# Kernel tuning notes

Measured on AMD Instinct MI355X. Metric: run time of the kernel, lower is better.

The kernel has to match this reference:

```python
import jax, jax.numpy as jnp
import numpy as np

RATIO_DENSE = 0.95   # ratio_th[-2] used for dense matching at conv5_2
RATIO_REFINE = 0.9   # ratio_th[k] used by refine_points
EPS = 1e-8
NEIGHBORS = jnp.array([[0, 0], [0, 1], [1, 0], [1, 1]])  # (x, y) offsets


def setup_inputs() -> dict:
    key = jax.random.key(0)
    k1, k2, k3, k4 = jax.random.split(key, 4)
    return {
        'map_A': jax.random.normal(k1, (1, 512, 96, 96), dtype=jnp.float32),
        'map_B': jax.random.normal(k2, (1, 512, 96, 96), dtype=jnp.float32),
        'act_A': jax.random.normal(k3, (1, 512, 192, 192), dtype=jnp.float32),
        'act_B': jax.random.normal(k4, (1, 512, 192, 192), dtype=jnp.float32),
    }


def _mnn_ratio_mask(sim, ratio):
    """Mutual-NN + ratio-test. sim: [N1, N2] cosine similarities.
    Returns nn12 [N1] (best match in B for each A) and boolean mask [N1]."""
    s12, i12 = jax.lax.top_k(sim, 2)            # [N1, 2]
    d12 = 2.0 - 2.0 * s12                       # cosine sim -> squared L2 dist
    r12 = d12[:, 0] / (d12[:, 1] + EPS)
    nn12 = i12[:, 0]
    s21, i21 = jax.lax.top_k(sim.T, 2)          # [N2, 2]
    d21 = 2.0 - 2.0 * s21
    r21 = d21[:, 0] / (d21[:, 1] + EPS)
    nn21 = i21[:, 0]
    ids1 = jnp.arange(sim.shape[0])
    mask = (ids1 == nn21[nn12]) & (r12 <= ratio) & (r21[nn12] <= ratio)
    return nn12, mask


def reference(map_A, map_B, act_A, act_B):
    ch = map_A.shape[1]
    hA, wA = map_A.shape[2], map_A.shape[3]
    hB, wB = map_B.shape[2], map_B.shape[3]

    # ---- dense_feature_matching (padded / masked form) ----
    d1 = map_A.reshape(ch, -1).T               # [N1, ch]
    d1 = d1 / jnp.linalg.norm(d1, axis=1, keepdims=True)
    d2 = map_B.reshape(ch, -1).T               # [N2, ch]
    d2 = d2 / jnp.linalg.norm(d2, axis=1, keepdims=True)
    sim = d1 @ d2.T                            # [N1, N2], the big one
    nn12, valid = _mnn_ratio_mask(sim, RATIO_DENSE)

    idx = jnp.arange(hA * wA)
    yA, xA = jnp.divmod(idx, wA)
    yB, xB = jnp.divmod(nn12, wB)
    border = ((xA == 0) | (xA == wA - 1) | (yA == 0) | (yA == hA - 1) |
              (xB == 0) | (xB == wB - 1) | (yB == 0) | (yB == hB - 1))
    valid = valid & ~border
    # pad invalid points to (0,0) so refine gathers stay in-bounds
    pA = jnp.stack([jnp.where(valid, xA, 0), jnp.where(valid, yA, 0)])  # [2, P]
    pB = jnp.stack([jnp.where(valid, xB, 0), jnp.where(valid, yB, 0)])

    # ---- refine_points (fully vectorized gather-dot-topk over all P points) ----
    dA = act_A[0] / jnp.sqrt(jnp.sum(act_A[0] ** 2, axis=0, keepdims=True))
    dB = act_B[0] / jnp.sqrt(jnp.sum(act_B[0] ** 2, axis=0, keepdims=True))
    pA2 = pA * 2
    pB2 = pB * 2
    P = pA.shape[1]

    gAx = pA2[0][:, None] + NEIGHBORS[:, 0][None, :]   # [P, 4]
    gAy = pA2[1][:, None] + NEIGHBORS[:, 1][None, :]
    gBx = pB2[0][:, None] + NEIGHBORS[:, 0][None, :]
    gBy = pB2[1][:, None] + NEIGHBORS[:, 1][None, :]
    actAg = dA[:, gAy, gAx]                            # [ch, P, 4]
    actBg = dB[:, gBy, gBx]                            # [ch, P, 4]
    scores = jnp.einsum('cpi,cpj->pij', actAg, actBg)  # [P, 4, 4]

    sA, mA = jax.lax.top_k(scores, 2)                  # [P, 4, 2]
    sA = 2.0 - 2.0 * sA
    ratio_A2B = sA[..., 0] / (sA[..., 1] + EPS)        # [P, 4]
    match_A2B = mA[..., 0]
    score_A2B = sA[..., 0]

    sB, mB = jax.lax.top_k(jnp.swapaxes(scores, 1, 2), 2)
    sB = 2.0 - 2.0 * sB
    ratio_B2A = sB[..., 0] / (sB[..., 1] + EPS)
    match_B2A = mB[..., 0]

    ar = jnp.arange(P)
    ind_A = (ar[:, None] * 4 + match_A2B).reshape(-1)  # [P*4]
    ind_B = (ar[:, None] * 4 + match_B2A).reshape(-1)
    ind = jnp.arange(P * 4)
    mask = (jnp.minimum(ratio_A2B, ratio_B2A) < RATIO_REFINE) & \
           (ind_B[ind_A] == ind).reshape(P, 4)

    # drop the two worst (largest-distance) neighbor candidates per point
    score_masked = jnp.where(mask, score_A2B, 5.0)
    _, discard = jax.lax.top_k(score_masked, 2)
    mask = mask.at[ar, discard[:, 0]].set(False)
    mask = mask.at[ar, discard[:, 1]].set(False)
    mask = mask & valid[:, None]

    refined_A = jnp.stack([gAx, gAy])                                   # [2, P, 4]
    rBx = pB2[0][:, None] + NEIGHBORS[:, 0][match_A2B]
    rBy = pB2[1][:, None] + NEIGHBORS[:, 1][match_A2B]
    refined_B = jnp.stack([rBx, rBy])                                   # [2, P, 4]

    return refined_A, refined_B, mask, scores
```

## Files before the change

### kernel.cpp

```cpp
#include <hip/hip_runtime.h>
#include <stdint.h>

#define CH 512
#define W1 96
#define P1 (W1*W1)
#define W2 192
#define P2 (W2*W2)
#define TILE 128
#define NT (P1/TILE)
#define BK 32
#define EPSF 1e-8f
#define RDENSE 0.95f
#define RREFINE 0.9f

typedef __attribute__((ext_vector_type(8))) short bf16x8_t;
typedef __attribute__((ext_vector_type(4))) float f32x4_t;

__device__ __forceinline__ unsigned enc_f32(float f){
  unsigned u = __float_as_uint(f);
  return (u & 0x80000000u) ? ~u : (u | 0x80000000u);
}
__device__ __forceinline__ float dec_f32(unsigned e){
  unsigned u = (e & 0x80000000u) ? (e & 0x7FFFFFFFu) : ~e;
  return __uint_as_float(u);
}
__device__ __forceinline__ unsigned long long packVI(float v, int idx){
  return (((unsigned long long)enc_f32(v)) << 32) | (unsigned)(~(unsigned)idx);
}
__device__ __forceinline__ float packedVal(unsigned long long p){ return dec_f32((unsigned)(p >> 32)); }
__device__ __forceinline__ int packedIdx(unsigned long long p){ return (int)(~(unsigned)(p & 0xFFFFFFFFull)); }
__device__ __forceinline__ void merge2(unsigned long long &b, unsigned long long &s, unsigned long long c){
  if (c > b){ s = b; b = c; } else if (c > s){ s = c; }
}

__device__ __forceinline__ unsigned short f2bf(float f){
  unsigned u = __float_as_uint(f);
  unsigned r = (u + 0x7FFFu + ((u >> 16) & 1u)) >> 16;
  return (unsigned short)r;
}

__device__ __forceinline__ void gload16(const void* g, void* l){
  __builtin_amdgcn_global_load_lds(
      (const __attribute__((address_space(1))) unsigned int*)g,
      (__attribute__((address_space(3))) unsigned int*)l, 16, 0, 0);
}

__global__ void desc_norm(const float* __restrict__ mA, const float* __restrict__ mB,
                          float* __restrict__ inv1, float* __restrict__ inv2){
  int p = blockIdx.x * blockDim.x + threadIdx.x;
  const float* m = (p < P1) ? mA : mB;
  float* o = (p < P1) ? inv1 : inv2;
  int pix = (p < P1) ? p : p - P1;
  float s = 0.f;
  for (int c = 0; c < CH; ++c){ float v = m[c*P1 + pix]; s += v*v; }
  o[pix] = 1.0f / sqrtf(s);
}

__global__ void act_norm(const float* __restrict__ aA, const float* __restrict__ aB,
                         float* __restrict__ invA, float* __restrict__ invB){
  int p = blockIdx.x * blockDim.x + threadIdx.x;
  const float* m = (p < P2) ? aA : aB;
  float* o = (p < P2) ? invA : invB;
  int pix = (p < P2) ? p : p - P2;
  float s = 0.f;
  for (int c = 0; c < CH; ++c){ float v = m[c*P2 + pix]; s += v*v; }
  o[pix] = 1.0f / sqrtf(s);
}

__global__ __launch_bounds__(256)
void prep_split(const float* __restrict__ src, const float* __restrict__ inv,
                unsigned short* __restrict__ hi, unsigned short* __restrict__ lo){
  __shared__ float tile[64][65];
  const int pixBase = blockIdx.x * 64;
  const int chBase  = blockIdx.y * 64;
  const int t = threadIdx.x;
  #pragma unroll
  for (int rep = 0; rep < 16; ++rep){
    int idx = rep*256 + t;
    int c = idx >> 6, p = idx & 63;
    tile[c][p] = src[(chBase + c)*P1 + pixBase + p];
  }
  __syncthreads();
  const int p = t >> 2, cg = (t & 3) * 16;
  const float iv = inv[pixBase + p];
  unsigned short hbuf[16], lbuf[16];
  #pragma unroll
  for (int j = 0; j < 16; ++j){
    float v = tile[cg + j][p] * iv;
    unsigned short h = f2bf(v);
    float hv = __uint_as_float((unsigned)h << 16);
    unsigned short l2 = f2bf(v - hv);
    hbuf[j] = h; lbuf[j] = l2;
  }
  size_t off = (size_t)(pixBase + p) * CH + chBase + cg;
  *(uint4*)(hi + off)     = ((const uint4*)hbuf)[0];
  *(uint4*)(hi + off + 8) = ((const uint4*)hbuf)[1];
  *(uint4*)(lo + off)     = ((const uint4*)lbuf)[0];
  *(uint4*)(lo + off + 8) = ((const uint4*)lbuf)[1];
}

__global__ __launch_bounds__(256, 2)
void sim_mfma(const unsigned short* __restrict__ Ah, const unsigned short* __restrict__ Al,
              const unsigned short* __restrict__ Bh, const unsigned short* __restrict__ Bl,
              unsigned long long* __restrict__ rowCand,
              unsigned long long* __restrict__ colCand){
  __shared__ unsigned short ldsT[4][TILE*BK];
  __shared__ unsigned long long rowScr[TILE][2][2];
  __shared__ unsigned long long colScr[TILE][2][2];

  const int nwg = NT*NT;
  int bid = blockIdx.x;
  int swz = (bid & 7) * (nwg >> 3) + (bid >> 3);
  const int rt = swz / NT, ct = swz % NT;
  const int rBase = rt * TILE, cBase = ct * TILE;

  const int t = threadIdx.x;
  const int w = t >> 6, lane = t & 63;
  const int wr = w >> 1, wc = w & 1;
  const int l15 = lane & 15, lj = lane >> 4;

  const unsigned short* panel = (w == 0) ? (Ah + (size_t)rBase*CH)
                              : (w == 1) ? (Al + (size_t)rBase*CH)
                              : (w == 2) ? (Bh + (size_t)cBase*CH)
                                         : (Bl + (size_t)cBase*CH);
  int srcOff[8];
  #pragma unroll
  for (int i = 0; i < 8; ++i){
    int slot = i*64 + lane;
    int row = slot >> 2, chkp = slot & 3;
    int chk = chkp ^ ((row >> 1) & 3);
    srcOff[i] = row * (CH*2) + chk * 16;
  }

  f32x4_t acc[4][4];
  #pragma unroll
  for (int i = 0; i < 4; ++i)
    #pragma unroll
    for (int j = 0; j < 4; ++j)
      #pragma unroll
      for (int r = 0; r < 4; ++r) acc[i][j][r] = 0.f;

  int aOff[4], bOff[4];
  #pragma unroll
  for (int mi = 0; mi < 4; ++mi){
    int rA = wr*64 + mi*16 + l15;
    aOff[mi] = rA*BK + ((lj ^ ((rA >> 1) & 3)) << 3);
  }
  #pragma unroll
  for (int ni = 0; ni < 4; ++ni){
    int rB = wc*64 + ni*16 + l15;
    bOff[ni] = rB*BK + ((lj ^ ((rB >> 1) & 3)) << 3);
  }

  for (int k0 = 0; k0 < CH; k0 += BK){
    const char* pbase = (const char*)panel + k0*2;
    unsigned short* mylds = &ldsT[w][0];
    #pragma unroll
    for (int i = 0; i < 8; ++i)
      gload16(pbase + srcOff[i], mylds + i*512);
    __syncthreads();

    bf16x8_t ah[4], al[4], bh[4], bl[4];
    #pragma unroll
    for (int mi = 0; mi < 4; ++mi){
      ah[mi] = *(const bf16x8_t*)&ldsT[0][aOff[mi]];
      al[mi] = *(const bf16x8_t*)&ldsT[1][aOff[mi]];
    }
    #pragma unroll
    for (int ni = 0; ni < 4; ++ni){
      bh[ni] = *(const bf16x8_t*)&ldsT[2][bOff[ni]];
      bl[ni] = *(const bf16x8_t*)&ldsT[3][bOff[ni]];
    }
    #pragma unroll
    for (int mi = 0; mi < 4; ++mi)
      #pragma unroll
      for (int ni = 0; ni < 4; ++ni){
        acc[mi][ni] = __builtin_amdgcn_mfma_f32_16x16x32_bf16(ah[mi], bh[ni], acc[mi][ni], 0, 0, 0);
        acc[mi][ni] = __builtin_amdgcn_mfma_f32_16x16x32_bf16(ah[mi], bl[ni], acc[mi][ni], 0, 0, 0);
        acc[mi][ni] = __builtin_amdgcn_mfma_f32_16x16x32_bf16(al[mi], bh[ni], acc[mi][ni], 0, 0, 0);
      }
    __syncthreads();
  }

  #pragma unroll
  for (int mi = 0; mi < 4; ++mi){
    #pragma unroll
    for (int reg = 0; reg < 4; ++reg){
      unsigned long long b = 0ull, s = 0ull;
      #pragma unroll
      for (int ni = 0; ni < 4; ++ni){
        int col = cBase + wc*64 + ni*16 + l15;
        merge2(b, s, packVI(acc[mi][ni][reg], col));
      }
      #pragma unroll
      for (int m = 1; m < 16; m <<= 1){
        unsigned long long ob = __shfl_xor(b, m, 64);
        unsigned long long os = __shfl_xor(s, m, 64);
        merge2(b, s, ob); merge2(b, s, os);
      }
      if (l15 == 0){
        int rowLoc = wr*64 + mi*16 + lj*4 + reg;
        rowScr[rowLoc][wc][0] = b; rowScr[rowLoc][wc][1] = s;
      }
    }
  }
  #pragma unroll
  for (int ni = 0; ni < 4; ++ni){
    unsigned long long b = 0ull, s = 0ull;
    #pragma unroll
    for (int mi = 0; mi < 4; ++mi)
      #pragma unroll
      for (int reg = 0; reg < 4; ++reg){
        int row = rBase + wr*64 + mi*16 + lj*4 + reg;
        merge2(b, s, packVI(acc[mi][ni][reg], row));
      }
    #pragma unroll
    for (int m = 16; m < 64; m <<= 1){
      unsigned long long ob = __shfl_xor(b, m, 64);
      unsigned long long os = __shfl_xor(s, m, 64);
      merge2(b, s, ob); merge2(b, s, os);
    }
    if (lj == 0){
      int colLoc = wc*64 + ni*16 + l15;
      colScr[colLoc][wr][0] = b; colScr[colLoc][wr][1] = s;
    }
  }
  __syncthreads();
  if (t < TILE){
    unsigned long long b = 0ull, s = 0ull;
    merge2(b, s, rowScr[t][0][0]); merge2(b, s, rowScr[t][0][1]);
    merge2(b, s, rowScr[t][1][0]); merge2(b, s, rowScr[t][1][1]);
    rowCand[((long long)ct*P1 + rBase + t)*2 + 0] = b;
    rowCand[((long long)ct*P1 + rBase + t)*2 + 1] = s;
  } else {
    int c = t - TILE;
    unsigned long long b = 0ull, s = 0ull;
    merge2(b, s, colScr[c][0][0]); merge2(b, s, colScr[c][0][1]);
    merge2(b, s, colScr[c][1][0]); merge2(b, s, colScr[c][1][1]);
    colCand[((long long)rt*P1 + cBase + c)*2 + 0] = b;
    colCand[((long long)rt*P1 + cBase + c)*2 + 1] = s;
  }
}

__global__ void merge_cand(const unsigned long long* __restrict__ cand,
                           unsigned long long* __restrict__ top,
                           unsigned long long* __restrict__ sec){
  int p = blockIdx.x * blockDim.x + threadIdx.x;
  unsigned long long b = 0ull, s = 0ull;
  for (int tile = 0; tile < NT; ++tile){
    merge2(b, s, cand[((long long)tile*P1 + p)*2 + 0]);
    merge2(b, s, cand[((long long)tile*P1 + p)*2 + 1]);
  }
  top[p] = b; sec[p] = s;
}

__global__ void match_k(const unsigned long long* __restrict__ rowTop,
                        const unsigned long long* __restrict__ rowSec,
                        const unsigned long long* __restrict__ colTop,
                        const unsigned long long* __restrict__ colSec,
                        int4* __restrict__ pts, int* __restrict__ validArr){
  int p = blockIdx.x * blockDim.x + threadIdx.x;
  unsigned long long rT = rowTop[p], rS = rowSec[p];
  float s0 = packedVal(rT), s1 = packedVal(rS);
  int nn12 = packedIdx(rT);
  float r12 = (2.f - 2.f*s0) / (2.f - 2.f*s1 + EPSF);
  unsigned long long cT = colTop[nn12], cS = colSec[nn12];
  int nn21 = packedIdx(cT);
  float r21 = (2.f - 2.f*packedVal(cT)) / (2.f - 2.f*packedVal(cS) + EPSF);
  int xA = p % W1, yA = p / W1, xB = nn12 % W1, yB = nn12 / W1;
  bool border = (xA==0)||(xA==W1-1)||(yA==0)||(yA==W1-1)||
                (xB==0)||(xB==W1-1)||(yB==0)||(yB==W1-1);
  bool valid = (nn21 == p) && (r12 <= RDENSE) && (r21 <= RDENSE) && !border;
  pts[p] = valid ? make_int4(xA,yA,xB,yB) : make_int4(0,0,0,0);
  validArr[p] = valid ? 1 : 0;
}

__global__ __launch_bounds__(256)
void refine(const float* __restrict__ actA, const float* __restrict__ actB,
            const float* __restrict__ invA, const float* __restrict__ invB,
            const int4* __restrict__ pts, float* __restrict__ scoresOut){
  int p = (blockIdx.x * blockDim.x + threadIdx.x) >> 6;
  int lane = threadIdx.x & 63;
  int4 q = pts[p];
  const int nbx[4] = {0,0,1,1}, nby[4] = {0,1,0,1};
  int offA[4], offB[4];
  #pragma unroll
  for (int i = 0; i < 4; ++i){
    offA[i] = (2*q.y + nby[i])*W2 + 2*q.x + nbx[i];
    offB[i] = (2*q.w + nby[i])*W2 + 2*q.z + nbx[i];
  }
  float acc[16] = {};
  #pragma unroll
  for (int k = 0; k < 8; ++k){
    int c = lane + 64*k;
    int base = c * P2;
    float a0 = actA[base+offA[0]], a1 = actA[base+offA[1]],
          a2 = actA[base+offA[2]], a3 = actA[base+offA[3]];
    float b0 = actB[base+offB[0]], b1 = actB[base+offB[1]],
          b2 = actB[base+offB[2]], b3 = actB[base+offB[3]];
    acc[ 0] = fmaf(a0,b0,acc[ 0]); acc[ 1] = fmaf(a0,b1,acc[ 1]);
    acc[ 2] = fmaf(a0,b2,acc[ 2]); acc[ 3] = fmaf(a0,b3,acc[ 3]);
    acc[ 4] = fmaf(a1,b0,acc[ 4]); acc[ 5] = fmaf(a1,b1,acc[ 5]);
    acc[ 6] = fmaf(a1,b2,acc[ 6]); acc[ 7] = fmaf(a1,b3,acc[ 7]);
    acc[ 8] = fmaf(a2,b0,acc[ 8]); acc[ 9] = fmaf(a2,b1,acc[ 9]);
    acc[10] = fmaf(a2,b2,acc[10]); acc[11] = fmaf(a2,b3,acc[11]);
    acc[12] = fmaf(a3,b0,acc[12]); acc[13] = fmaf(a3,b1,acc[13]);
    acc[14] = fmaf(a3,b2,acc[14]); acc[15] = fmaf(a3,b3,acc[15]);
  }
  #pragma unroll
  for (int m = 1; m < 64; m <<= 1)
    #pragma unroll
    for (int u = 0; u < 16; ++u) acc[u] += __shfl_xor(acc[u], m, 64);
  if (lane == 0){
    float sA[4], sB[4];
    #pragma unroll
    for (int i = 0; i < 4; ++i){ sA[i] = invA[offA[i]]; sB[i] = invB[offB[i]]; }
    float4* o = (float4*)(scoresOut + p*16);
    #pragma unroll
    for (int i = 0; i < 4; ++i)
      o[i] = make_float4(acc[i*4+0]*sA[i]*sB[0], acc[i*4+1]*sA[i]*sB[1],
                         acc[i*4+2]*sA[i]*sB[2], acc[i*4+3]*sA[i]*sB[3]);
  }
}

__global__ void final_k(const float* __restrict__ scores, const int4* __restrict__ pts,
                        const int* __restrict__ validArr, float* __restrict__ out){
  int p = blockIdx.x * blockDim.x + threadIdx.x;
  float sc[16];
  #pragma unroll
  for (int u = 0; u < 16; ++u) sc[u] = scores[p*16 + u];

  int matchA[4]; float ratioA[4], scoreA[4];
  #pragma unroll
  for (int i = 0; i < 4; ++i){
    int bi = 0; float bv = sc[i*4];
    #pragma unroll
    for (int j = 1; j < 4; ++j) if (sc[i*4+j] > bv){ bv = sc[i*4+j]; bi = j; }
    float sv = -3.402823466e38f;
    #pragma unroll
    for (int j = 0; j < 4; ++j) if (j != bi && sc[i*4+j] > sv){ sv = sc[i*4+j]; }
    matchA[i] = bi;
    float d0 = 2.f - 2.f*bv, d1 = 2.f - 2.f*sv;
    ratioA[i] = d0 / (d1 + EPSF); scoreA[i] = d0;
  }
  int matchB[4]; float ratioB[4];
  #pragma unroll
  for (int j = 0; j < 4; ++j){
    int bi = 0; float bv = sc[j];
    #pragma unroll
    for (int i = 1; i < 4; ++i) if (sc[i*4+j] > bv){ bv = sc[i*4+j]; bi = i; }
    float sv = -3.402823466e38f;
    #pragma unroll
    for (int i = 0; i < 4; ++i) if (i != bi && sc[i*4+j] > sv){ sv = sc[i*4+j]; }
    matchB[j] = bi;
    float d0 = 2.f - 2.f*bv, d1 = 2.f - 2.f*sv;
    ratioB[j] = d0 / (d1 + EPSF);
  }
  bool m[4];
  #pragma unroll
  for (int i = 0; i < 4; ++i)
    m[i] = (fminf(ratioA[i], ratioB[i]) < RREFINE) && (matchB[matchA[i]] == i);
  float smk[4];
  #pragma unroll
  for (int i = 0; i < 4; ++i) smk[i] = m[i] ? scoreA[i] : 5.0f;
  int d0i = 0; float d0v = smk[0];
  #pragma unroll
  for (int i = 1; i < 4; ++i) if (smk[i] > d0v){ d0v = smk[i]; d0i = i; }
  int d1i = -1; float d1v = -3.402823466e38f;
  #pragma unroll
  for (int i = 0; i < 4; ++i) if (i != d0i && smk[i] > d1v){ d1v = smk[i]; d1i = i; }
  m[d0i] = false; m[d1i] = false;
  bool v = validArr[p] != 0;
  int4 q = pts[p];
  const int nbx[4] = {0,0,1,1}, nby[4] = {0,1,0,1};
  #pragma unroll
  for (int i = 0; i < 4; ++i){
    out[           p*4 + i] = (float)(2*q.x + nbx[i]);
    out[  P1*4   + p*4 + i] = (float)(2*q.y + nby[i]);
    out[2*P1*4   + p*4 + i] = (float)(2*q.z + nbx[matchA[i]]);
    out[3*P1*4   + p*4 + i] = (float)(2*q.w + nby[matchA[i]]);
    out[4*P1*4   + p*4 + i] = (m[i] && v) ? 1.0f : 0.0f;
  }
}

extern "C" void kernel_launch(void* const* d_in, const int* in_sizes, int n_in,
                              void* d_out, int out_size, void* d_ws, size_t ws_size,
                              hipStream_t stream) {
  const float* mapA = (const float*)d_in[0];
  const float* mapB = (const float*)d_in[1];
  const float* actA = (const float*)d_in[2];
  const float* actB = (const float*)d_in[3];
  float* out = (float*)d_out;

  unsigned short* Ah = (unsigned short*)d_ws;
  unsigned short* Al = Ah + (size_t)P1*CH;
  unsigned short* Bh = Al + (size_t)P1*CH;
  unsigned short* Bl = Bh + (size_t)P1*CH;
  unsigned long long* rowCand = (unsigned long long*)(Bl + (size_t)P1*CH);
  unsigned long long* colCand = rowCand + (size_t)NT*P1*2;
  unsigned long long* rowTop  = colCand + (size_t)NT*P1*2;
  unsigned long long* rowSec  = rowTop + P1;
  unsigned long long* colTop  = rowSec + P1;
  unsigned long long* colSec  = colTop + P1;
  float* inv1 = (float*)(colSec + P1);
  float* inv2 = inv1 + P1;
  float* invA = inv2 + P1;
  float* invB = invA + P2;
  int4*  pts  = (int4*)(invB + P2);
  int*   validArr = (int*)(pts + P1);

  float* scoresOut = out + 4*P1*4 + P1*4;

  desc_norm <<<2*P1/256, 256, 0, stream>>>(mapA, mapB, inv1, inv2);
  act_norm  <<<2*P2/256, 256, 0, stream>>>(actA, actB, invA, invB);
  prep_split<<<dim3(P1/64, CH/64), 256, 0, stream>>>(mapA, inv1, Ah, Al);
  prep_split<<<dim3(P1/64, CH/64), 256, 0, stream>>>(mapB, inv2, Bh, Bl);
  sim_mfma  <<<NT*NT, 256, 0, stream>>>(Ah, Al, Bh, Bl, rowCand, colCand);
  merge_cand<<<P1/256, 256, 0, stream>>>(rowCand, rowTop, rowSec);
  merge_cand<<<P1/256, 256, 0, stream>>>(colCand, colTop, colSec);
  match_k   <<<P1/256, 256, 0, stream>>>(rowTop, rowSec, colTop, colSec, pts, validArr);
  refine    <<<P1*64/256, 256, 0, stream>>>(actA, actB, invA, invB, pts, scoresOut);
  final_k   <<<P1/256, 256, 0, stream>>>(scoresOut, pts, validArr, out);
}
```

Baseline: 1.670 ms.

## Enlarge similarity GEMM tile to 256x256 with double-buffered LDS prefetch

The split-bf16 similarity GEMM grows from 128x128 tiles with 4 waves to 256x256 tiles with 8 waves. Each wave now computes 128x64 instead of 64x64. The per-k-step LDS staging is double-buffered, so the next K slice's global-to-LDS loads are issued while the current slice runs its MFMAs. This is meant to cut global/L2 traffic per FLOP and hide load latency. The cost is a 128KB LDS footprint, which likely limits each CU to one workgroup, plus more accumulator registers and fewer workgroups in the grid. The top-2 candidate merge logic and buffer sizes are adjusted to the new tile count.

```diff
diff --git a/kernel.cpp b/kernel.cpp
--- a/kernel.cpp
+++ b/kernel.cpp
@@ -6,9 +6,11 @@
 #define P1 (W1*W1)
 #define W2 192
 #define P2 (W2*W2)
-#define TILE 128
-#define NT (P1/TILE)
+#define BM 256
+#define BN 256
+#define NTT 36
 #define BK 32
+#define NKS (CH/BK)
 #define EPSF 1e-8f
 #define RDENSE 0.95f
 #define RREFINE 0.9f
@@ -99,91 +101,101 @@
   *(uint4*)(lo + off + 8) = ((const uint4*)lbuf)[1];
 }
 
-__global__ __launch_bounds__(256, 2)
+__global__ __launch_bounds__(512, 2)
 void sim_mfma(const unsigned short* __restrict__ Ah, const unsigned short* __restrict__ Al,
               const unsigned short* __restrict__ Bh, const unsigned short* __restrict__ Bl,
               unsigned long long* __restrict__ rowCand,
               unsigned long long* __restrict__ colCand){
-  __shared__ unsigned short ldsT[4][TILE*BK];
-  __shared__ unsigned long long rowScr[TILE][2][2];
-  __shared__ unsigned long long colScr[TILE][2][2];
-
-  const int nwg = NT*NT;
+  __shared__ __align__(16) char lds[131072];
+
+  const int nwg = NTT*NTT;
   int bid = blockIdx.x;
   int swz = (bid & 7) * (nwg >> 3) + (bid >> 3);
-  const int rt = swz / NT, ct = swz % NT;
-  const int rBase = rt * TILE, cBase = ct * TILE;
+  const int rt = swz / NTT, ct = swz % NTT;
+  const int rBase = rt * BM, cBase = ct * BN;
 
   const int t = threadIdx.x;
   const int w = t >> 6, lane = t & 63;
-  const int wr = w >> 1, wc = w & 1;
+  const int wr = w >> 2, wc = w & 3;
   const int l15 = lane & 15, lj = lane >> 4;
 
-  const unsigned short* panel = (w == 0) ? (Ah + (size_t)rBase*CH)
-                              : (w == 1) ? (Al + (size_t)rBase*CH)
-                              : (w == 2) ? (Bh + (size_t)cBase*CH)
-                                         : (Bl + (size_t)cBase*CH);
-  int srcOff[8];
+  const int panel = w >> 1, sub = w & 1;
+  const unsigned short* gpan = (panel == 0) ? (Ah + (size_t)rBase*CH)
+                             : (panel == 1) ? (Al + (size_t)rBase*CH)
+                             : (panel == 2) ? (Bh + (size_t)cBase*CH)
+                                            : (Bl + (size_t)cBase*CH);
+  int gOff[8];
   #pragma unroll
   for (int i = 0; i < 8; ++i){
-    int slot = i*64 + lane;
+    int slot = sub*512 + i*64 + lane;
     int row = slot >> 2, chkp = slot & 3;
     int chk = chkp ^ ((row >> 1) & 3);
-    srcOff[i] = row * (CH*2) + chk * 16;
-  }
-
-  f32x4_t acc[4][4];
-  #pragma unroll
-  for (int i = 0; i < 4; ++i)
-    #pragma unroll
-    for (int j = 0; j < 4; ++j)
-      #pragma unroll
-      for (int r = 0; r < 4; ++r) acc[i][j][r] = 0.f;
-
-  int aOff[4], bOff[4];
-  #pragma unroll
-  for (int mi = 0; mi < 4; ++mi){
-    int rA = wr*64 + mi*16 + l15;
-    aOff[mi] = rA*BK + ((lj ^ ((rA >> 1) & 3)) << 3);
+    gOff[i] = row * (CH*2) + chk * 16;
+  }
+  const int ldsPanelOff = panel*16384 + sub*8192;
+
+  int aOff[8], bOff[4];
+  #pragma unroll
+  for (int mi = 0; mi < 8; ++mi){
+    int rA = wr*128 + mi*16 + l15;
+    aOff[mi] = rA*64 + ((lj ^ ((rA >> 1) & 3)) << 4);
   }
   #pragma unroll
   for (int ni = 0; ni < 4; ++ni){
     int rB = wc*64 + ni*16 + l15;
-    bOff[ni] = rB*BK + ((lj ^ ((rB >> 1) & 3)) << 3);
-  }
-
-  for (int k0 = 0; k0 < CH; k0 += BK){
-    const char* pbase = (const char*)panel + k0*2;
-    unsigned short* mylds = &ldsT[w][0];
+    bOff[ni] = rB*64 + ((lj ^ ((rB >> 1) & 3)) << 4);
+  }
+
+  f32x4_t acc[8][4];
+  #pragma unroll
+  for (int i = 0; i < 8; ++i)
+    #pragma unroll
+    for (int j = 0; j < 4; ++j)
+      #pragma unroll
+      for (int r = 0; r < 4; ++r) acc[i][j][r] = 0.f;
+
+  {
+    const char* gb = (const char*)gpan;
     #pragma unroll
     for (int i = 0; i < 8; ++i)
-      gload16(pbase + srcOff[i], mylds + i*512);
+      gload16(gb + gOff[i], lds + ldsPanelOff + i*1024);
+  }
+  __syncthreads();
+
+  for (int ks = 0; ks < NKS; ++ks){
+    const int cur = ks & 1;
+    if (ks + 1 < NKS){
+      const char* gb = (const char*)gpan + (ks+1)*BK*2;
+      #pragma unroll
+      for (int i = 0; i < 8; ++i)
+        gload16(gb + gOff[i], lds + (cur^1)*65536 + ldsPanelOff + i*1024);
+    }
+    const char* bp = lds + cur*65536;
+    bf16x8_t ahf[8], alf[8];
+    #pragma unroll
+    for (int mi = 0; mi < 8; ++mi){
+      ahf[mi] = *(const bf16x8_t*)(bp + aOff[mi]);
+      alf[mi] = *(const bf16x8_t*)(bp + 16384 + aOff[mi]);
+    }
+    #pragma unroll
+    for (int ni = 0; ni < 4; ++ni){
+      bf16x8_t bhf = *(const bf16x8_t*)(bp + 32768 + bOff[ni]);
+      bf16x8_t blf = *(const bf16x8_t*)(bp + 49152 + bOff[ni]);
+      #pragma unroll
+      for (int mi = 0; mi < 8; ++mi){
+        acc[mi][ni] = __builtin_amdgcn_mfma_f32_16x16x32_bf16(ahf[mi], bhf, acc[mi][ni], 0, 0, 0);
+        acc[mi][ni] = __builtin_amdgcn_mfma_f32_16x16x32_bf16(ahf[mi], blf, acc[mi][ni], 0, 0, 0);
+        acc[mi][ni] = __builtin_amdgcn_mfma_f32_16x16x32_bf16(alf[mi], bhf, acc[mi][ni], 0, 0, 0);
+      }
+    }
     __syncthreads();
-
-    bf16x8_t ah[4], al[4], bh[4], bl[4];
-    #pragma unroll
-    for (int mi = 0; mi < 4; ++mi){
-      ah[mi] = *(const bf16x8_t*)&ldsT[0][aOff[mi]];
-      al[mi] = *(const bf16x8_t*)&ldsT[1][aOff[mi]];
-    }
-    #pragma unroll
-    for (int ni = 0; ni < 4; ++ni){
-      bh[ni] = *(const bf16x8_t*)&ldsT[2][bOff[ni]];
-      bl[ni] = *(const bf16x8_t*)&ldsT[3][bOff[ni]];
-    }
-    #pragma unroll
-    for (int mi = 0; mi < 4; ++mi)
-      #pragma unroll
-      for (int ni = 0; ni < 4; ++ni){
-        acc[mi][ni] = __builtin_amdgcn_mfma_f32_16x16x32_bf16(ah[mi], bh[ni], acc[mi][ni], 0, 0, 0);
-        acc[mi][ni] = __builtin_amdgcn_mfma_f32_16x16x32_bf16(ah[mi], bl[ni], acc[mi][ni], 0, 0, 0);
-        acc[mi][ni] = __builtin_amdgcn_mfma_f32_16x16x32_bf16(al[mi], bh[ni], acc[mi][ni], 0, 0, 0);
-      }
-    __syncthreads();
-  }
-
-  #pragma unroll
-  for (int mi = 0; mi < 4; ++mi){
+  }
+
+  unsigned long long (*rowScr)[4][2] = (unsigned long long (*)[4][2])(lds);
+  unsigned long long (*colScr)[2][2] = (unsigned long long (*)[2][2])(lds + 16384);
+
+  #pragma unroll
+  for (int mi = 0; mi < 8; ++mi){
     #pragma unroll
     for (int reg = 0; reg < 4; ++reg){
       unsigned long long b = 0ull, s = 0ull;
@@ -199,7 +211,7 @@
         merge2(b, s, ob); merge2(b, s, os);
       }
       if (l15 == 0){
-        int rowLoc = wr*64 + mi*16 + lj*4 + reg;
+        int rowLoc = wr*128 + mi*16 + lj*4 + reg;
         rowScr[rowLoc][wc][0] = b; rowScr[rowLoc][wc][1] = s;
       }
     }
@@ -208,10 +220,10 @@
   for (int ni = 0; ni < 4; ++ni){
     unsigned long long b = 0ull, s = 0ull;
     #pragma unroll
-    for (int mi = 0; mi < 4; ++mi)
+    for (int mi = 0; mi < 8; ++mi)
       #pragma unroll
       for (int reg = 0; reg < 4; ++reg){
-        int row = rBase + wr*64 + mi*16 + lj*4 + reg;
+        int row = rBase + wr*128 + mi*16 + lj*4 + reg;
         merge2(b, s, packVI(acc[mi][ni][reg], row));
       }
     #pragma unroll
@@ -226,17 +238,17 @@
     }
   }
   __syncthreads();
-  if (t < TILE){
+  if (t < 256){
     unsigned long long b = 0ull, s = 0ull;
-    merge2(b, s, rowScr[t][0][0]); merge2(b, s, rowScr[t][0][1]);
-    merge2(b, s, rowScr[t][1][0]); merge2(b, s, rowScr[t][1][1]);
+    #pragma unroll
+    for (int j = 0; j < 4; ++j){ merge2(b, s, rowScr[t][j][0]); merge2(b, s, rowScr[t][j][1]); }
     rowCand[((long long)ct*P1 + rBase + t)*2 + 0] = b;
     rowCand[((long long)ct*P1 + rBase + t)*2 + 1] = s;
   } else {
-    int c = t - TILE;
+    int c = t - 256;
     unsigned long long b = 0ull, s = 0ull;
-    merge2(b, s, colScr[c][0][0]); merge2(b, s, colScr[c][0][1]);
-    merge2(b, s, colScr[c][1][0]); merge2(b, s, colScr[c][1][1]);
+    #pragma unroll
+    for (int j = 0; j < 2; ++j){ merge2(b, s, colScr[c][j][0]); merge2(b, s, colScr[c][j][1]); }
     colCand[((long long)rt*P1 + cBase + c)*2 + 0] = b;
     colCand[((long long)rt*P1 + cBase + c)*2 + 1] = s;
   }
@@ -247,7 +259,7 @@
                            unsigned long long* __restrict__ sec){
   int p = blockIdx.x * blockDim.x + threadIdx.x;
   unsigned long long b = 0ull, s = 0ull;
-  for (int tile = 0; tile < NT; ++tile){
+  for (int tile = 0; tile < NTT; ++tile){
     merge2(b, s, cand[((long long)tile*P1 + p)*2 + 0]);
     merge2(b, s, cand[((long long)tile*P1 + p)*2 + 1]);
   }
@@ -397,8 +409,8 @@
   unsigned short* Bh = Al + (size_t)P1*CH;
   unsigned short* Bl = Bh + (size_t)P1*CH;
   unsigned long long* rowCand = (unsigned long long*)(Bl + (size_t)P1*CH);
-  unsigned long long* colCand = rowCand + (size_t)NT*P1*2;
-  unsigned long long* rowTop  = colCand + (size_t)NT*P1*2;
+  unsigned long long* colCand = rowCand + (size_t)NTT*P1*2;
+  unsigned long long* rowTop  = colCand + (size_t)NTT*P1*2;
   unsigned long long* rowSec  = rowTop + P1;
   unsigned long long* colTop  = rowSec + P1;
   unsigned long long* colSec  = colTop + P1;
@@ -415,7 +427,7 @@
   act_norm  <<<2*P2/256, 256, 0, stream>>>(actA, actB, invA, invB);
   prep_split<<<dim3(P1/64, CH/64), 256, 0, stream>>>(mapA, inv1, Ah, Al);
   prep_split<<<dim3(P1/64, CH/64), 256, 0, stream>>>(mapB, inv2, Bh, Bl);
-  sim_mfma  <<<NT*NT, 256, 0, stream>>>(Ah, Al, Bh, Bl, rowCand, colCand);
+  sim_mfma  <<<NTT*NTT, 512, 0, stream>>>(Ah, Al, Bh, Bl, rowCand, colCand);
   merge_cand<<<P1/256, 256, 0, stream>>>(rowCand, rowTop, rowSec);
   merge_cand<<<P1/256, 256, 0, stream>>>(colCand, colTop, colSec);
   match_k   <<<P1/256, 256, 0, stream>>>(rowTop, rowSec, colTop, colSec, pts, validArr);
```

After: 1.762 ms. 1.06x slower.
